# Performance work log

Measured on AMD Instinct MI355X. Metric: run time of the kernel, lower is better.

Reference implementation:

```python
import jax, jax.numpy as jnp
import numpy as np

NUM_HEADS = 16
NEG = -1e9

def setup_inputs() -> dict:
    key = jax.random.key(0)
    ks = jax.random.split(key, 5)
    B, S, D = 4, 2048, 1024
    scale = 1.0 / np.sqrt(D)
    return {
        "x": jax.random.normal(ks[0], (B, S, D), dtype=jnp.float32),
        "WQ": jax.random.normal(ks[1], (D, D), dtype=jnp.float32) * scale,
        "WK": jax.random.normal(ks[2], (D, D), dtype=jnp.float32) * scale,
        "WV": jax.random.normal(ks[3], (D, D), dtype=jnp.float32) * scale,
        "WO": jax.random.normal(ks[4], (D, D), dtype=jnp.float32) * scale,
    }

def _split_heads(t, h):
    # [..., s, h*d] -> [..., h, s, d]
    *lead, s, hd = t.shape
    return jnp.swapaxes(t.reshape(*lead, s, h, hd // h), -3, -2)

def reference(x, WQ, WK, WV, WO):
    h = NUM_HEADS
    S = x.shape[-2]
    # Linear stores weight [out, in]; y = x @ W^T
    Q = _split_heads(x @ WQ.T, h)  # [b,h,s,dk]
    K = _split_heads(x @ WK.T, h)
    V = _split_heads(x @ WV.T, h)
    dk = Q.shape[-1]
    scores = jnp.einsum('bhqd,bhkd->bhqk', Q, K) / jnp.sqrt(jnp.float32(dk))
    causal = jnp.tril(jnp.ones((S, S), dtype=bool))  # allowed positions
    scores = jnp.where(causal, scores, NEG)
    # explicit stable softmax (matches source)
    m = jnp.max(scores, axis=-1, keepdims=True)
    e = jnp.exp(scores - m)
    attn = e / jnp.sum(e, axis=-1, keepdims=True)
    out = jnp.einsum('bhqk,bhkd->bhqd', attn, V)  # [b,h,s,dv]
    out = jnp.swapaxes(out, -3, -2).reshape(*x.shape[:-1], -1)  # [b,s,h*dv]
    return out @ WO.T
```

## Files before the change

kernel.cpp:

```cpp
#include <hip/hip_runtime.h>
#include <stdint.h>
#include <math.h>

typedef __attribute__((ext_vector_type(8))) short bf16x8;
typedef __attribute__((ext_vector_type(4))) short v4s;
typedef __attribute__((ext_vector_type(4))) float f32x4;
typedef __attribute__((ext_vector_type(4))) unsigned short u16x4;
typedef __attribute__((ext_vector_type(2))) unsigned int u32x2;

#define MFMA16(a,b,c)   __builtin_amdgcn_mfma_f32_16x16x32_bf16((a),(b),(c),0,0,0)
#define MFMA16K(a,b,c)  __builtin_amdgcn_mfma_f32_16x16x16bf16_1k((a),(b),(c),0,0,0)

static __device__ __forceinline__ void gld_lds16(const void* g, void* l) {
  __builtin_amdgcn_global_load_lds(
      (const __attribute__((address_space(1))) unsigned int*)g,
      (__attribute__((address_space(3))) unsigned int*)l,
      16, 0, 0);
}

static __device__ __forceinline__ unsigned short f2bf(float f) {
  unsigned int u = __builtin_bit_cast(unsigned int, f);
  return (unsigned short)((u + 0x8000u) >> 16);
}

__global__ __launch_bounds__(256) void cvt_kernel(const float* __restrict__ in,
                                                  unsigned short* __restrict__ out,
                                                  int n4) {
  int i = blockIdx.x * blockDim.x + threadIdx.x;
  int stride = gridDim.x * blockDim.x;
  for (; i < n4; i += stride) {
    float4 v = ((const float4*)in)[i];
    u16x4 o;
    o.x = f2bf(v.x); o.y = f2bf(v.y); o.z = f2bf(v.z); o.w = f2bf(v.w);
    ((u16x4*)out)[i] = o;
  }
}

__global__ __launch_bounds__(256) void cvt4_kernel(const float* __restrict__ w0,
                                                   const float* __restrict__ w1,
                                                   const float* __restrict__ w2,
                                                   const float* __restrict__ w3,
                                                   unsigned short* __restrict__ out) {
  const float* in = (blockIdx.y == 0) ? w0 : (blockIdx.y == 1) ? w1
                  : (blockIdx.y == 2) ? w2 : w3;
  unsigned short* o = out + (size_t)blockIdx.y * 1048576;
  int i = blockIdx.x * blockDim.x + threadIdx.x;
  int stride = gridDim.x * blockDim.x;
  for (; i < 1048576/4; i += stride) {
    float4 v = ((const float4*)in)[i];
    u16x4 t;
    t.x = f2bf(v.x); t.y = f2bf(v.y); t.z = f2bf(v.z); t.w = f2bf(v.w);
    ((u16x4*)o)[i] = t;
  }
}

template<int MODE, typename CT>
__device__ __forceinline__ void gemm_bt_tile(const unsigned short* __restrict__ A,
                                             const unsigned short* __restrict__ Bt,
                                             CT* __restrict__ C,
                                             int m0, int n0,
                                             unsigned short* As,
                                             unsigned short* Bs)
{
  const int tid  = threadIdx.x;
  const int w    = tid >> 6, lane = tid & 63;
  const int quad = lane >> 4, c0 = lane & 15;
  const int wm   = w >> 1, wn = w & 1;

  const unsigned short* ga[2];
  const unsigned short* gb[2];
  int ldsoff[2];
  #pragma unroll
  for (int i = 0; i < 2; ++i) {
    int f = i*4096 + w*1024 + lane*16;
    int r = f >> 6;
    int q = (f >> 4) & 3;
    int gq = q ^ ((r >> 1) & 3);
    ga[i] = A  + (m0 + r)*1024 + gq*8;
    gb[i] = Bt + (n0 + r)*1024 + gq*8;
    ldsoff[i] = i*4096 + w*1024;
  }

  int aAddr[4], bAddr[4];
  const int sq = (quad ^ ((c0 >> 1) & 3)) * 16;
  #pragma unroll
  for (int t = 0; t < 4; ++t) {
    aAddr[t] = (wm*64 + t*16 + c0)*64 + sq;
    bAddr[t] = (wn*64 + t*16 + c0)*64 + sq;
  }

  f32x4 acc[4][4];
  #pragma unroll
  for (int i = 0; i < 4; ++i)
    #pragma unroll
    for (int j = 0; j < 4; ++j)
      acc[i][j] = (f32x4){0.f, 0.f, 0.f, 0.f};

  for (int kt = 0; kt < 32; ++kt) {
    __syncthreads();
    #pragma unroll
    for (int i = 0; i < 2; ++i) {
      gld_lds16(ga[i] + kt*32, (char*)As + ldsoff[i]);
      gld_lds16(gb[i] + kt*32, (char*)Bs + ldsoff[i]);
    }
    __syncthreads();

    bf16x8 af[4], bfr[4];
    #pragma unroll
    for (int t = 0; t < 4; ++t) af[t]  = *(const bf16x8*)((const char*)As + aAddr[t]);
    #pragma unroll
    for (int t = 0; t < 4; ++t) bfr[t] = *(const bf16x8*)((const char*)Bs + bAddr[t]);

    #pragma unroll
    for (int mt = 0; mt < 4; ++mt)
      #pragma unroll
      for (int nt = 0; nt < 4; ++nt)
        acc[mt][nt] = MFMA16(af[mt], bfr[nt], acc[mt][nt]);
  }

  const float scl = (MODE == 3) ? 0.1803368801f : 1.0f;
  #pragma unroll
  for (int mt = 0; mt < 4; ++mt) {
    #pragma unroll
    for (int nt = 0; nt < 4; ++nt) {
      if (MODE == 2) {
        u16x4 pk;
        #pragma unroll
        for (int r = 0; r < 4; ++r) pk[r] = f2bf(acc[mt][nt][r]);
        int s0 = m0 + wm*64 + mt*16 + quad*4;
        int gc = n0 + wn*64 + nt*16 + c0;
        int b = s0 >> 11, ss = s0 & 2047;
        int h = gc >> 6, d = gc & 63;
        *(u16x4*)((unsigned short*)C + (size_t)(((b << 4) + h)*64 + d)*2048 + ss) = pk;
      } else {
        #pragma unroll
        for (int r = 0; r < 4; ++r) {
          int gr = m0 + wm*64 + mt*16 + quad*4 + r;
          int gc = n0 + wn*64 + nt*16 + c0;
          if (MODE == 0 || MODE == 3) {
            int b = gr >> 11, s = gr & 2047;
            int h = gc >> 6, d = gc & 63;
            ((unsigned short*)C)[(((b << 4) + h)*2048 + s)*64 + d] = f2bf(acc[mt][nt][r] * scl);
          } else {
            ((float*)C)[gr*1024 + gc] = acc[mt][nt][r];
          }
        }
      }
    }
  }
}

__global__ __launch_bounds__(256) void qkv_kernel(
    const unsigned short* __restrict__ X,
    const unsigned short* __restrict__ WQ, const unsigned short* __restrict__ WK,
    const unsigned short* __restrict__ WV,
    unsigned short* __restrict__ Q, unsigned short* __restrict__ K,
    unsigned short* __restrict__ V)
{
  __shared__ __align__(16) unsigned short As[128*32];
  __shared__ __align__(16) unsigned short Bs[128*32];
  if (blockIdx.z == 2) {
    gemm_bt_tile<2>(X, WV, V, blockIdx.x*128, blockIdx.y*128, As, Bs);
  } else if (blockIdx.z == 0) {
    gemm_bt_tile<3>(X, WQ, Q, blockIdx.x*128, blockIdx.y*128, As, Bs);
  } else {
    gemm_bt_tile<0>(X, WK, K, blockIdx.x*128, blockIdx.y*128, As, Bs);
  }
}

__global__ __launch_bounds__(256) void proj_kernel(
    const unsigned short* __restrict__ A,
    const unsigned short* __restrict__ WO,
    float* __restrict__ C)
{
  __shared__ __align__(16) unsigned short As[128*32];
  __shared__ __align__(16) unsigned short Bs[128*32];
  gemm_bt_tile<1>(A, WO, C, blockIdx.x*128, blockIdx.y*128, As, Bs);
}

__global__ __launch_bounds__(256, 2) void attn_kernel(
    const unsigned short* __restrict__ Q,
    const unsigned short* __restrict__ K,
    const unsigned short* __restrict__ Vt,
    unsigned short* __restrict__ O)
{
  __shared__ __align__(16) unsigned short VtL[2][64*128];
  __shared__ __align__(16) unsigned short KL[2][128*64];

  const int tid  = threadIdx.x;
  const int w    = tid >> 6, lane = tid & 63;
  const int quad = lane >> 4, c0 = lane & 15;
  const int bx = blockIdx.y, bh = blockIdx.x;

  const unsigned short* Qh = Q  + (size_t)bh*2048*64;
  const unsigned short* Kh = K  + (size_t)bh*2048*64;
  const unsigned short* Vh = Vt + (size_t)bh*64*2048;

  const unsigned short* vga[4];
  const unsigned short* kga[4];
  int ldso[4];
  #pragma unroll
  for (int i = 0; i < 4; ++i) {
    int cid = i*256 + tid;
    int vr = cid >> 4, vq = cid & 15;
    vga[i] = Vh + (size_t)vr*2048 + (vq ^ (vr & 15))*8;
    int kr = cid >> 3, kq = cid & 7;
    kga[i] = Kh + (size_t)kr*64 + (kq ^ (kr & 7))*8;
    ldso[i] = i*4096 + w*1024;
  }

  const int b = bh >> 4, h = bh & 15;

  #define ATTN_MK_BODY(mk, Kb, Vb, DIAG)                                          \
  {                                                                               \
    bf16x8 ka0 = *(const bf16x8*)((const char*)(Kb) + ((mk)*16 + c0)*128          \
                                  + (((0*4 + quad) ^ (c0 & 7)) * 16));            \
    bf16x8 ka1 = *(const bf16x8*)((const char*)(Kb) + ((mk)*16 + c0)*128          \
                                  + (((1*4 + quad) ^ (c0 & 7)) * 16));            \
    f32x4 s0 = (f32x4){0.f,0.f,0.f,0.f}, s1 = (f32x4){0.f,0.f,0.f,0.f};           \
    s0 = MFMA16(ka0, qf[0][0], s0);                                               \
    s1 = MFMA16(ka0, qf[1][0], s1);                                               \
    s0 = MFMA16(ka1, qf[0][1], s0);                                               \
    s1 = MFMA16(ka1, qf[1][1], s1);                                               \
    if (DIAG) {                                                                   \
      _Pragma("unroll")                                                           \
      for (int r = 0; r < 4; ++r) {                                               \
        int kk = (mk)*16 + quad*4 + r;                                            \
        if (kk > w*32 + c0)      s0[r] = -1e30f;                                  \
        if (kk > w*32 + 16 + c0) s1[r] = -1e30f;                                  \
      }                                                                           \
    }                                                                             \
    float p00 = __builtin_amdgcn_exp2f(s0[0]), p01 = __builtin_amdgcn_exp2f(s0[1]); \
    float p02 = __builtin_amdgcn_exp2f(s0[2]), p03 = __builtin_amdgcn_exp2f(s0[3]); \
    float p10 = __builtin_amdgcn_exp2f(s1[0]), p11 = __builtin_amdgcn_exp2f(s1[1]); \
    float p12 = __builtin_amdgcn_exp2f(s1[2]), p13 = __builtin_amdgcn_exp2f(s1[3]); \
    l_r[0] += (p00 + p01) + (p02 + p03);                                          \
    l_r[1] += (p10 + p11) + (p12 + p13);                                          \
    u32x2 a0, a1;                                                                 \
    a0.x = __builtin_amdgcn_perm(__builtin_bit_cast(unsigned int, p01),           \
                                 __builtin_bit_cast(unsigned int, p00), 0x07060302u); \
    a0.y = __builtin_amdgcn_perm(__builtin_bit_cast(unsigned int, p03),           \
                                 __builtin_bit_cast(unsigned int, p02), 0x07060302u); \
    a1.x = __builtin_amdgcn_perm(__builtin_bit_cast(unsigned int, p11),           \
                                 __builtin_bit_cast(unsigned int, p10), 0x07060302u); \
    a1.y = __builtin_amdgcn_perm(__builtin_bit_cast(unsigned int, p13),           \
                                 __builtin_bit_cast(unsigned int, p12), 0x07060302u); \
    v4s pa0 = __builtin_bit_cast(v4s, a0);                                        \
    v4s pa1 = __builtin_bit_cast(v4s, a1);                                        \
    _Pragma("unroll")                                                             \
    for (int dt = 0; dt < 4; ++dt) {                                              \
      int vr = dt*16 + c0;                                                        \
      int p  = 2*(mk) + (quad >> 1);                                              \
      v4s vb = *(const v4s*)((const char*)(Vb) + vr*256 + ((p ^ c0) * 16) + (quad & 1)*8); \
      o_[0][dt] = MFMA16K(pa0, vb, o_[0][dt]);                                    \
      o_[1][dt] = MFMA16K(pa1, vb, o_[1][dt]);                                    \
    }                                                                             \
  }

  for (int pi = 0; pi < 2; ++pi) {
    const int qt = pi ? bx : 15 - bx;

    bf16x8 qf[2][2];
    #pragma unroll
    for (int mq = 0; mq < 2; ++mq)
      #pragma unroll
      for (int ks = 0; ks < 2; ++ks)
        qf[mq][ks] = *(const bf16x8*)(Qh + (qt*128 + w*32 + mq*16 + c0)*64 + ks*32 + quad*8);

    f32x4 o_[2][4];
    float l_r[2] = {0.f, 0.f};
    #pragma unroll
    for (int mq = 0; mq < 2; ++mq)
      #pragma unroll
      for (int dt = 0; dt < 4; ++dt) o_[mq][dt] = (f32x4){0.f, 0.f, 0.f, 0.f};

    __syncthreads();
    #pragma unroll
    for (int i = 0; i < 4; ++i) {
      gld_lds16(vga[i], (char*)VtL[0] + ldso[i]);
      gld_lds16(kga[i], (char*)KL[0]  + ldso[i]);
    }

    for (int kt = 0; kt < qt; ++kt) {
      __syncthreads();
      #pragma unroll
      for (int i = 0; i < 4; ++i) {
        gld_lds16(vga[i] + (kt+1)*128,  (char*)VtL[(kt+1)&1] + ldso[i]);
        gld_lds16(kga[i] + (kt+1)*8192, (char*)KL[(kt+1)&1]  + ldso[i]);
      }
      const unsigned short* Vb = VtL[kt & 1];
      const unsigned short* Kb = KL[kt & 1];
      __builtin_amdgcn_s_setprio(1);
      #pragma unroll
      for (int mk = 0; mk < 8; ++mk)
        ATTN_MK_BODY(mk, Kb, Vb, false)
      __builtin_amdgcn_s_setprio(0);
    }

    {
      __syncthreads();
      const unsigned short* Vb = VtL[qt & 1];
      const unsigned short* Kb = KL[qt & 1];
      __builtin_amdgcn_s_setprio(1);
      #pragma unroll
      for (int mk = 0; mk < 8; ++mk)
        if (mk < 2*w + 2)
          ATTN_MK_BODY(mk, Kb, Vb, true)
      __builtin_amdgcn_s_setprio(0);
    }

    #pragma unroll
    for (int mq = 0; mq < 2; ++mq) {
      l_r[mq] += __shfl_xor(l_r[mq], 16);
      l_r[mq] += __shfl_xor(l_r[mq], 32);
    }
    #pragma unroll
    for (int mt = 0; mt < 2; ++mt) {
      #pragma unroll
      for (int r = 0; r < 4; ++r) {
        float l = __shfl(l_r[mt], quad*4 + r);
        float inv = 1.0f / l;
        int srow = qt*128 + w*32 + mt*16 + quad*4 + r;
        #pragma unroll
        for (int dt = 0; dt < 4; ++dt) {
          int col = h*64 + dt*16 + c0;
          O[((size_t)b*2048 + srow)*1024 + col] = f2bf(o_[mt][dt][r] * inv);
        }
      }
    }
  }
  #undef ATTN_MK_BODY
}

extern "C" void kernel_launch(void* const* d_in, const int* in_sizes, int n_in,
                              void* d_out, int out_size, void* d_ws, size_t ws_size,
                              hipStream_t stream) {
  const float* xf  = (const float*)d_in[0];
  const float* wqf = (const float*)d_in[1];
  const float* wkf = (const float*)d_in[2];
  const float* wvf = (const float*)d_in[3];
  const float* wof = (const float*)d_in[4];
  float* out = (float*)d_out;
  unsigned short* ws = (unsigned short*)d_ws;

  const bool fused = ws_size >= (size_t)58720256;

  if (fused) {
    unsigned short* xb  = ws;
    unsigned short* wb  = ws + 8388608;
    unsigned short* Kw  = ws + 12582912;
    unsigned short* Vw  = ws + 20971520;
    unsigned short* Ow  = xb;
    unsigned short* Qd  = (unsigned short*)out;

    cvt_kernel <<<2048, 256, 0, stream>>>(xf, xb, 8388608/4);
    cvt4_kernel<<<dim3(256, 4), 256, 0, stream>>>(wqf, wkf, wvf, wof, wb);

    qkv_kernel <<<dim3(64, 8, 3), 256, 0, stream>>>(xb, wb, wb + 1048576, wb + 2097152,
                                                    Qd, Kw, Vw);
    attn_kernel<<<dim3(64, 8),    256, 0, stream>>>(Qd, Kw, Vw, Ow);
    proj_kernel<<<dim3(64, 8),    256, 0, stream>>>(Ow, wb + 3145728, out);
  } else {
    unsigned short* xb  = ws;
    unsigned short* wb  = ws + 8388608;
    unsigned short* Kw  = ws + 12582912;
    unsigned short* Vw  = ws + 14680064;
    unsigned short* Ow  = ws + 16777216;

    cvt_kernel <<<2048, 256, 0, stream>>>(xf, xb, 8388608/4);
    cvt4_kernel<<<dim3(256, 4), 256, 0, stream>>>(wqf, wkf, wvf, wof, wb);

    for (int b = 0; b < 4; ++b) {
      const unsigned short* xbb = xb  + (size_t)b * 2048 * 1024;
      float*               outb = out + (size_t)b * 2048 * 1024;
      unsigned short*        Qd = (unsigned short*)outb;
      qkv_kernel <<<dim3(16, 8, 3), 256, 0, stream>>>(xbb, wb, wb + 1048576, wb + 2097152,
                                                      Qd, Kw, Vw);
      attn_kernel<<<dim3(16, 8),    256, 0, stream>>>(Qd, Kw, Vw, Ow);
      proj_kernel<<<dim3(16, 8),    256, 0, stream>>>(Ow, wb + 3145728, outb);
    }
  }
}
```

Measured before the change: 251.6 us.

## Fuse Q/K/V projections into one kernel sharing the X tile

```diff
diff --git a/kernel.cpp b/kernel.cpp
--- a/kernel.cpp
+++ b/kernel.cpp
@@ -54,6 +54,102 @@
   }
 }
 
+__global__ __launch_bounds__(512, 2) void qkv_fused_kernel(
+    const unsigned short* __restrict__ X,
+    const unsigned short* __restrict__ WQ, const unsigned short* __restrict__ WK,
+    const unsigned short* __restrict__ WV,
+    unsigned short* __restrict__ Q, unsigned short* __restrict__ K,
+    unsigned short* __restrict__ V)
+{
+  __shared__ __align__(16) unsigned short Xs[128*32];
+  __shared__ __align__(16) unsigned short Ws0[128*32];
+  __shared__ __align__(16) unsigned short Ws1[128*32];
+  __shared__ __align__(16) unsigned short Ws2[128*32];
+
+  const int tid  = threadIdx.x;
+  const int w    = tid >> 6, lane = tid & 63;
+  const int quad = lane >> 4, c0 = lane & 15;
+  const int wm   = w >> 1, wn = w & 1;
+  const int m0 = blockIdx.x * 128, n0 = blockIdx.y * 128;
+
+  const int r  = tid >> 2, q = tid & 3;
+  const int gq = q ^ ((r >> 1) & 3);
+  const unsigned short* gx  = X  + (m0 + r)*1024 + gq*8;
+  const unsigned short* gw0 = WQ + (n0 + r)*1024 + gq*8;
+  const unsigned short* gw1 = WK + (n0 + r)*1024 + gq*8;
+  const unsigned short* gw2 = WV + (n0 + r)*1024 + gq*8;
+  const int lb = w * 1024;
+
+  int aAddr[2], bAddr[4];
+  const int sq = (quad ^ ((c0 >> 1) & 3)) * 16;
+  #pragma unroll
+  for (int t = 0; t < 2; ++t) aAddr[t] = (wm*32 + t*16 + c0)*64 + sq;
+  #pragma unroll
+  for (int t = 0; t < 4; ++t) bAddr[t] = (wn*64 + t*16 + c0)*64 + sq;
+
+  f32x4 aQ[2][4], aK[2][4], aV[2][4];
+  #pragma unroll
+  for (int i = 0; i < 2; ++i)
+    #pragma unroll
+    for (int j = 0; j < 4; ++j) {
+      aQ[i][j] = (f32x4){0.f, 0.f, 0.f, 0.f};
+      aK[i][j] = (f32x4){0.f, 0.f, 0.f, 0.f};
+      aV[i][j] = (f32x4){0.f, 0.f, 0.f, 0.f};
+    }
+
+  for (int kt = 0; kt < 32; ++kt) {
+    __syncthreads();
+    gld_lds16(gx  + kt*32, (char*)Xs  + lb);
+    gld_lds16(gw0 + kt*32, (char*)Ws0 + lb);
+    gld_lds16(gw1 + kt*32, (char*)Ws1 + lb);
+    gld_lds16(gw2 + kt*32, (char*)Ws2 + lb);
+    __syncthreads();
+
+    bf16x8 af[2], bq[4], bk[4], bv[4];
+    #pragma unroll
+    for (int t = 0; t < 2; ++t) af[t] = *(const bf16x8*)((const char*)Xs  + aAddr[t]);
+    #pragma unroll
+    for (int t = 0; t < 4; ++t) bq[t] = *(const bf16x8*)((const char*)Ws0 + bAddr[t]);
+    #pragma unroll
+    for (int t = 0; t < 4; ++t) bk[t] = *(const bf16x8*)((const char*)Ws1 + bAddr[t]);
+    #pragma unroll
+    for (int t = 0; t < 4; ++t) bv[t] = *(const bf16x8*)((const char*)Ws2 + bAddr[t]);
+
+    #pragma unroll
+    for (int mt = 0; mt < 2; ++mt)
+      #pragma unroll
+      for (int nt = 0; nt < 4; ++nt) {
+        aQ[mt][nt] = MFMA16(af[mt], bq[nt], aQ[mt][nt]);
+        aK[mt][nt] = MFMA16(af[mt], bk[nt], aK[mt][nt]);
+        aV[mt][nt] = MFMA16(af[mt], bv[nt], aV[mt][nt]);
+      }
+  }
+
+  const float scl = 0.1803368801f;
+  #pragma unroll
+  for (int mt = 0; mt < 2; ++mt) {
+    #pragma unroll
+    for (int nt = 0; nt < 4; ++nt) {
+      int gc = n0 + wn*64 + nt*16 + c0;
+      int hh = gc >> 6, d = gc & 63;
+      #pragma unroll
+      for (int r4 = 0; r4 < 4; ++r4) {
+        int gr = m0 + wm*32 + mt*16 + quad*4 + r4;
+        int b = gr >> 11, s = gr & 2047;
+        size_t base = ((size_t)(((b << 4) + hh)*2048 + s))*64 + d;
+        Q[base] = f2bf(aQ[mt][nt][r4] * scl);
+        K[base] = f2bf(aK[mt][nt][r4]);
+      }
+      u16x4 pk;
+      #pragma unroll
+      for (int r4 = 0; r4 < 4; ++r4) pk[r4] = f2bf(aV[mt][nt][r4]);
+      int s0 = m0 + wm*32 + mt*16 + quad*4;
+      int b = s0 >> 11, ss = s0 & 2047;
+      *(u16x4*)(V + ((size_t)(((b << 4) + hh)*64 + d))*2048 + ss) = pk;
+    }
+  }
+}
+
 template<int MODE, typename CT>
 __device__ __forceinline__ void gemm_bt_tile(const unsigned short* __restrict__ A,
                                              const unsigned short* __restrict__ Bt,
@@ -118,53 +214,17 @@
         acc[mt][nt] = MFMA16(af[mt], bfr[nt], acc[mt][nt]);
   }
 
-  const float scl = (MODE == 3) ? 0.1803368801f : 1.0f;
   #pragma unroll
   for (int mt = 0; mt < 4; ++mt) {
     #pragma unroll
     for (int nt = 0; nt < 4; ++nt) {
-      if (MODE == 2) {
-        u16x4 pk;
-        #pragma unroll
-        for (int r = 0; r < 4; ++r) pk[r] = f2bf(acc[mt][nt][r]);
-        int s0 = m0 + wm*64 + mt*16 + quad*4;
+      #pragma unroll
+      for (int r = 0; r < 4; ++r) {
+        int gr = m0 + wm*64 + mt*16 + quad*4 + r;
         int gc = n0 + wn*64 + nt*16 + c0;
-        int b = s0 >> 11, ss = s0 & 2047;
-        int h = gc >> 6, d = gc & 63;
-        *(u16x4*)((unsigned short*)C + (size_t)(((b << 4) + h)*64 + d)*2048 + ss) = pk;
-      } else {
-        #pragma unroll
-        for (int r = 0; r < 4; ++r) {
-          int gr = m0 + wm*64 + mt*16 + quad*4 + r;
-          int gc = n0 + wn*64 + nt*16 + c0;
-          if (MODE == 0 || MODE == 3) {
-            int b = gr >> 11, s = gr & 2047;
-            int h = gc >> 6, d = gc & 63;
-            ((unsigned short*)C)[(((b << 4) + h)*2048 + s)*64 + d] = f2bf(acc[mt][nt][r] * scl);
-          } else {
-            ((float*)C)[gr*1024 + gc] = acc[mt][nt][r];
-          }
-        }
+        ((float*)C)[gr*1024 + gc] = acc[mt][nt][r];
       }
     }
-  }
-}
-
-__global__ __launch_bounds__(256) void qkv_kernel(
-    const unsigned short* __restrict__ X,
-    const unsigned short* __restrict__ WQ, const unsigned short* __restrict__ WK,
-    const unsigned short* __restrict__ WV,
-    unsigned short* __restrict__ Q, unsigned short* __restrict__ K,
-    unsigned short* __restrict__ V)
-{
-  __shared__ __align__(16) unsigned short As[128*32];
-  __shared__ __align__(16) unsigned short Bs[128*32];
-  if (blockIdx.z == 2) {
-    gemm_bt_tile<2>(X, WV, V, blockIdx.x*128, blockIdx.y*128, As, Bs);
-  } else if (blockIdx.z == 0) {
-    gemm_bt_tile<3>(X, WQ, Q, blockIdx.x*128, blockIdx.y*128, As, Bs);
-  } else {
-    gemm_bt_tile<0>(X, WK, K, blockIdx.x*128, blockIdx.y*128, As, Bs);
   }
 }
 
@@ -356,8 +416,8 @@
     cvt_kernel <<<2048, 256, 0, stream>>>(xf, xb, 8388608/4);
     cvt4_kernel<<<dim3(256, 4), 256, 0, stream>>>(wqf, wkf, wvf, wof, wb);
 
-    qkv_kernel <<<dim3(64, 8, 3), 256, 0, stream>>>(xb, wb, wb + 1048576, wb + 2097152,
-                                                    Qd, Kw, Vw);
+    qkv_fused_kernel<<<dim3(64, 8), 512, 0, stream>>>(xb, wb, wb + 1048576,
+                                                      wb + 2097152, Qd, Kw, Vw);
     attn_kernel<<<dim3(64, 8),    256, 0, stream>>>(Qd, Kw, Vw, Ow);
     proj_kernel<<<dim3(64, 8),    256, 0, stream>>>(Ow, wb + 3145728, out);
   } else {
@@ -374,8 +434,8 @@
       const unsigned short* xbb = xb  + (size_t)b * 2048 * 1024;
       float*               outb = out + (size_t)b * 2048 * 1024;
       unsigned short*        Qd = (unsigned short*)outb;
-      qkv_kernel <<<dim3(16, 8, 3), 256, 0, stream>>>(xbb, wb, wb + 1048576, wb + 2097152,
-                                                      Qd, Kw, Vw);
+      qkv_fused_kernel<<<dim3(16, 8), 512, 0, stream>>>(xbb, wb, wb + 1048576,
+                                                        wb + 2097152, Qd, Kw, Vw);
       attn_kernel<<<dim3(16, 8),    256, 0, stream>>>(Qd, Kw, Vw, Ow);
       proj_kernel<<<dim3(16, 8),    256, 0, stream>>>(Ow, wb + 3145728, outb);
     }
```

Measured after the change: 256.1 us. No clear change (+1.8%).
